# Optimization experiments

Measured on AMD Instinct MI355X. Metric: run time of the kernel, lower is better.

The kernel has to match this reference:

```python
import jax, jax.numpy as jnp
import numpy as np

B, T, V, E, H = 32, 64, 32000, 256, 512


def setup_inputs() -> dict:
    key = jax.random.key(0)
    ks = jax.random.split(key, 6)
    g = lambda k, shp, s: (jax.random.normal(k, shp, dtype=jnp.float32) * s)
    return {
        "trg": jax.random.randint(ks[0], (B, T), 0, V),
        "h0": g(ks[1], (1, B, H), 0.1),
        "embed_table": g(ks[2], (V, E), 0.02),
        "W_ih": g(ks[3], (3 * H, E), 0.05),
        "W_hh": g(ks[4], (3 * H, H), 0.05),
        "b_ih": jnp.zeros((3 * H,), jnp.float32),
        "b_hh": jnp.zeros((3 * H,), jnp.float32),
        "W_proj": g(ks[5], (V, H), 0.02),
        "b_proj": jnp.zeros((V,), jnp.float32),
    }


def _gru_decode(trg, h0, embed_table, W_ih, W_hh, b_ih, b_hh, W_proj, b_proj):
    # Teacher forcing with tf_ratio=1.0 (deterministic): token at step t is trg[:, t-1].
    Bd, Td = trg.shape
    Vd = W_proj.shape[0]
    emb = embed_table[trg[:, :-1]]                         # [B, T-1, E]
    # Precompute input-side gate projections for all steps at once.
    x_gates = jnp.einsum('bte,ge->btg', emb, W_ih) + b_ih  # [B, T-1, 3H]

    def step(h, xg):
        hg = h @ W_hh.T + b_hh                             # [B, 3H]
        xr, xz, xn = jnp.split(xg, 3, axis=-1)
        hr, hz, hn = jnp.split(hg, 3, axis=-1)
        r = jax.nn.sigmoid(xr + hr)
        z = jax.nn.sigmoid(xz + hz)
        n = jnp.tanh(xn + r * hn)
        h_new = (1.0 - z) * n + z * h                      # PyTorch GRU update
        logits = h_new @ W_proj.T + b_proj                 # [B, V]
        return h_new, jax.nn.log_softmax(logits, axis=-1)

    _, logps = jax.lax.scan(step, h0[0], jnp.swapaxes(x_gates, 0, 1))  # [T-1, B, V]
    out = jnp.concatenate(
        [jnp.zeros((Bd, 1, Vd), logps.dtype), jnp.swapaxes(logps, 0, 1)], axis=1
    )                                                      # out[:, 0] = 0 as in torch
    return out


def reference(trg, h0, embed_table, W_ih, W_hh, b_ih, b_hh, W_proj, b_proj):
    return _gru_decode(trg, h0, embed_table, W_ih, W_hh, b_ih, b_hh, W_proj, b_proj)
```

## Files before the change

### kernel.cpp

```cpp
#include <hip/hip_runtime.h>
#include <stdint.h>

#define B_  32
#define T_  64
#define V_  32000
#define E_  256
#define H_  512
#define TS  63

typedef __attribute__((ext_vector_type(8))) short short8;
typedef __attribute__((ext_vector_type(4))) float floatx4;

union U16c { uint4 u; short8 s; };

__device__ __forceinline__ short8 ld8(const unsigned short* p) {
    U16c x; x.u = *(const uint4*)p; return x.s;
}

__device__ __forceinline__ unsigned short f2bf(float f) {
    union { float f; unsigned u; } v; v.f = f;
    unsigned r = v.u + 0x7FFFu + ((v.u >> 16) & 1u);
    return (unsigned short)(r >> 16);
}

__global__ void k_cvt_wp(const float* __restrict__ wp, unsigned short* __restrict__ dst) {
    int i = blockIdx.x * blockDim.x + threadIdx.x;
    const float4* s = (const float4*)wp + (size_t)i * 2;
    float4 a = s[0], b = s[1];
    union { uint4 u; unsigned short h[8]; } o;
    o.h[0] = f2bf(a.x); o.h[1] = f2bf(a.y); o.h[2] = f2bf(a.z); o.h[3] = f2bf(a.w);
    o.h[4] = f2bf(b.x); o.h[5] = f2bf(b.y); o.h[6] = f2bf(b.z); o.h[7] = f2bf(b.w);
    ((uint4*)dst)[i] = o.u;
}

__global__ void k_setup(const float* __restrict__ wih, const float* __restrict__ whh,
                        const float* __restrict__ embt, const int* __restrict__ trg,
                        const float* __restrict__ h0,
                        unsigned short* __restrict__ wih_bf, unsigned short* __restrict__ whh_bf,
                        unsigned short* __restrict__ emb_bf, unsigned short* __restrict__ hall,
                        unsigned long long* __restrict__ hall64)
{
    const int NIH  = (3 * H_ * E_) / 4;
    const int NHH  = (3 * H_ * H_) / 4;
    const int NEMB = TS * B_ * E_ / 4;
    const int NPAD = 32 * E_ / 8;
    const int NH0  = B_ * H_ / 4;
    const int NZ   = 63 * B_ * 256 * 8 / 16;
    int i = blockIdx.x * blockDim.x + threadIdx.x;
    if (i < NIH + NHH) {
        const float* src; unsigned short* dst; int j;
        if (i < NIH) { src = wih; dst = wih_bf; j = i; }
        else         { src = whh; dst = whh_bf; j = i - NIH; }
        float4 v = ((const float4*)src)[j];
        union { unsigned long long u; unsigned short h[4]; } o;
        o.h[0] = f2bf(v.x); o.h[1] = f2bf(v.y); o.h[2] = f2bf(v.z); o.h[3] = f2bf(v.w);
        ((unsigned long long*)dst)[j] = o.u;
        return;
    }
    i -= NIH + NHH;
    if (i < NEMB) {
        int r = i >> 6, c = i & 63;
        int tt = r >> 5, b = r & 31;
        int tok = trg[b * T_ + tt];
        float4 v = ((const float4*)(embt + (size_t)tok * E_))[c];
        union { unsigned long long u; unsigned short h[4]; } o;
        o.h[0] = f2bf(v.x); o.h[1] = f2bf(v.y); o.h[2] = f2bf(v.z); o.h[3] = f2bf(v.w);
        ((unsigned long long*)(emb_bf + (size_t)r * E_))[c] = o.u;
        return;
    }
    i -= NEMB;
    if (i < NPAD) {
        uint4 z; z.x = z.y = z.z = z.w = 0u;
        ((uint4*)(emb_bf + (size_t)(TS * B_) * E_))[i] = z;
        return;
    }
    i -= NPAD;
    if (i < NH0) {
        float4 v = ((const float4*)h0)[i];
        unsigned pk01 = (unsigned)f2bf(v.x) | ((unsigned)f2bf(v.y) << 16);
        unsigned pk23 = (unsigned)f2bf(v.z) | ((unsigned)f2bf(v.w) << 16);
        union { unsigned long long u; unsigned h[2]; } o;
        o.h[0] = pk01; o.h[1] = pk23;
        ((unsigned long long*)hall)[i] = o.u;
        uint4 tw; tw.x = pk01; tw.y = 0u; tw.z = pk23; tw.w = 0u;
        ((uint4*)hall64)[i] = tw;
        return;
    }
    i -= NH0;
    if (i < NZ) {
        uint4 z; z.x = z.y = z.z = z.w = 0u;
        ((uint4*)(hall64 + (size_t)B_ * 256))[i] = z;
        return;
    }
}

__global__ __launch_bounds__(256) void k_xg(const unsigned short* __restrict__ A,
                                            const unsigned short* __restrict__ Bm,
                                            const float* __restrict__ bias,
                                            float* __restrict__ out)
{
    __shared__ unsigned short As[128 * 32];
    __shared__ unsigned short Bs[128 * 32];
    int m0 = blockIdx.x * 128, n0 = blockIdx.y * 128;
    int tid = threadIdx.x;
    int lane = tid & 63, w = tid >> 6;
    int wm = (w & 1) * 64, wn = (w >> 1) * 64;
    int row = lane & 15, quad = lane >> 4;
    int srow = lane >> 2, skc = lane & 3;
    floatx4 acc[4][4];
    #pragma unroll
    for (int a = 0; a < 4; ++a)
        #pragma unroll
        for (int b = 0; b < 4; ++b) acc[a][b] = (floatx4){0.f, 0.f, 0.f, 0.f};

    for (int k0 = 0; k0 < E_; k0 += 32) {
        if (k0) __syncthreads();
        #pragma unroll
        for (int p = 0; p < 2; ++p) {
            int seg = w * 2 + p;
            int m = seg * 16 + srow;
            __builtin_amdgcn_global_load_lds(
                (const __attribute__((address_space(1))) void*)(A + (size_t)(m0 + m) * E_ + k0 + skc * 8),
                (__attribute__((address_space(3))) void*)(As + seg * 512),
                16, 0, 0);
            __builtin_amdgcn_global_load_lds(
                (const __attribute__((address_space(1))) void*)(Bm + (size_t)(n0 + m) * E_ + k0 + skc * 8),
                (__attribute__((address_space(3))) void*)(Bs + seg * 512),
                16, 0, 0);
        }
        __syncthreads();
        short8 af[4], bf[4];
        #pragma unroll
        for (int mi2 = 0; mi2 < 4; ++mi2)
            af[mi2] = ld8(As + (wm + mi2 * 16 + row) * 32 + quad * 8);
        #pragma unroll
        for (int ni = 0; ni < 4; ++ni)
            bf[ni] = ld8(Bs + (wn + ni * 16 + row) * 32 + quad * 8);
        #pragma unroll
        for (int mi2 = 0; mi2 < 4; ++mi2)
            #pragma unroll
            for (int ni = 0; ni < 4; ++ni)
                acc[mi2][ni] = __builtin_amdgcn_mfma_f32_16x16x32_bf16(af[mi2], bf[ni], acc[mi2][ni], 0, 0, 0);
    }
    #pragma unroll
    for (int ni = 0; ni < 4; ++ni) {
        int n = n0 + wn + ni * 16 + row;
        float bp = bias[n];
        #pragma unroll
        for (int mi2 = 0; mi2 < 4; ++mi2) {
            #pragma unroll
            for (int v = 0; v < 4; ++v) {
                int m = m0 + wm + mi2 * 16 + quad * 4 + v;
                out[(size_t)m * 1536 + n] = acc[mi2][ni][v] + bp;
            }
        }
    }
}

__global__ __launch_bounds__(512) void k_gru(
    const unsigned short* __restrict__ whh_bf, const float* __restrict__ gx,
    const float* __restrict__ bhh, const float* __restrict__ h0,
    unsigned short* __restrict__ hall, unsigned long long* __restrict__ hall64)
{
    __shared__ unsigned short hs[32 * 528];
    __shared__ float gh[32][52];
    int blk = blockIdx.x, tid = threadIdx.x;
    int lane = tid & 63, w = tid >> 6;
    int mi = w & 1, gi = w >> 1;
    int row = lane & 15, quad = lane >> 4;
    int eb = tid >> 4, jl = tid & 15;
    int j = blk * 16 + jl;

    float bhhr = bhh[j], bhhz = bhh[H_ + j], bhhn = bhh[2*H_ + j];
    float hcur = h0[eb * H_ + j];

    short8 barr[16];
    if (w < 6) {
        int gr = gi * H_ + blk * 16 + row;
        const unsigned short* wrow = whh_bf + (size_t)gr * H_;
        #pragma unroll
        for (int kk = 0; kk < 16; ++kk)
            barr[kk] = ld8(wrow + kk * 32 + quad * 8);
    }

    for (int t = 0; t < TS; ++t) {
        const float* gxp = gx + (size_t)(t * B_ + eb) * 1536 + j;
        float xr = gxp[0], xz = gxp[512], xn = gxp[1024];

        const unsigned long long* src = hall64 + (size_t)t * (B_ * 256);
        unsigned long long wv[16];
        unsigned want = (unsigned)t;
        for (;;) {
            #pragma unroll
            for (int i = 0; i < 16; ++i)
                wv[i] = __hip_atomic_load(src + i * 512 + tid,
                                          __ATOMIC_RELAXED, __HIP_MEMORY_SCOPE_AGENT);
            bool ok = true;
            #pragma unroll
            for (int i = 0; i < 16; ++i) ok &= ((unsigned)(wv[i] >> 32) == want);
            if (ok) break;
        }
        #pragma unroll
        for (int i = 0; i < 16; ++i) {
            int idx = i * 512 + tid;
            ((unsigned*)(hs + (size_t)(idx >> 8) * 528))[idx & 255] = (unsigned)wv[i];
        }
        __syncthreads();

        if (w < 6) {
            floatx4 ah = {0.f, 0.f, 0.f, 0.f};
            int b_ = mi * 16 + row;
            #pragma unroll
            for (int kk = 0; kk < 16; ++kk)
                ah = __builtin_amdgcn_mfma_f32_16x16x32_bf16(
                        ld8(hs + b_ * 528 + kk * 32 + quad * 8), barr[kk], ah, 0, 0, 0);
            int cb = mi * 16 + quad * 4;
            int cn = gi * 16 + row;
            #pragma unroll
            for (int v = 0; v < 4; ++v) gh[cb + v][cn] = ah[v];
        }
        __syncthreads();
        {
            float hr = gh[eb][jl], hz = gh[eb][16 + jl], hn = gh[eb][32 + jl];
            float r = 1.f / (1.f + __expf(-(xr + hr + bhhr)));
            float z = 1.f / (1.f + __expf(-(xz + hz + bhhz)));
            float nn = tanhf(xn + r * (hn + bhhn));
            hcur = (1.f - z) * nn + z * hcur;
            float hnb = __shfl_xor(hcur, 1);
            if (!(tid & 1)) {
                unsigned pk = (unsigned)f2bf(hcur) | ((unsigned)f2bf(hnb) << 16);
                unsigned long long tw = ((unsigned long long)(unsigned)(t + 1) << 32) | pk;
                __hip_atomic_store(hall64 + ((size_t)(t + 1) * B_ + eb) * 256 + (j >> 1),
                                   tw, __ATOMIC_RELAXED, __HIP_MEMORY_SCOPE_AGENT);
                ((unsigned*)hall)[((size_t)(t + 1) * B_ + eb) * 256 + (j >> 1)] = pk;
            }
        }
    }
}

__global__ __launch_bounds__(256) void k_gemm(const unsigned short* __restrict__ A,
                                              const unsigned short* __restrict__ Bm,
                                              const float* __restrict__ bias,
                                              float* __restrict__ out)
{
    __shared__ unsigned short As[128 * 32];
    __shared__ unsigned short Bs[128 * 32];
    int m0 = blockIdx.x * 128, n0 = blockIdx.y * 128;
    int tid = threadIdx.x;
    int lane = tid & 63, w = tid >> 6;
    int wm = (w & 1) * 64, wn = (w >> 1) * 64;
    int row = lane & 15, quad = lane >> 4;
    int srow = lane >> 2, skc = lane & 3;
    floatx4 acc[4][4];
    #pragma unroll
    for (int a = 0; a < 4; ++a)
        #pragma unroll
        for (int b = 0; b < 4; ++b) acc[a][b] = (floatx4){0.f, 0.f, 0.f, 0.f};

    for (int k0 = 0; k0 < H_; k0 += 32) {
        if (k0) __syncthreads();
        #pragma unroll
        for (int p = 0; p < 2; ++p) {
            int seg = w * 2 + p;
            int m = seg * 16 + srow;
            __builtin_amdgcn_global_load_lds(
                (const __attribute__((address_space(1))) void*)(A + (size_t)(m0 + m) * H_ + k0 + skc * 8),
                (__attribute__((address_space(3))) void*)(As + seg * 512),
                16, 0, 0);
            __builtin_amdgcn_global_load_lds(
                (const __attribute__((address_space(1))) void*)(Bm + (size_t)(n0 + m) * H_ + k0 + skc * 8),
                (__attribute__((address_space(3))) void*)(Bs + seg * 512),
                16, 0, 0);
        }
        __syncthreads();
        short8 af[4], bf[4];
        #pragma unroll
        for (int mi2 = 0; mi2 < 4; ++mi2)
            af[mi2] = ld8(As + (wm + mi2 * 16 + row) * 32 + quad * 8);
        #pragma unroll
        for (int ni = 0; ni < 4; ++ni)
            bf[ni] = ld8(Bs + (wn + ni * 16 + row) * 32 + quad * 8);
        #pragma unroll
        for (int mi2 = 0; mi2 < 4; ++mi2)
            #pragma unroll
            for (int ni = 0; ni < 4; ++ni)
                acc[mi2][ni] = __builtin_amdgcn_mfma_f32_16x16x32_bf16(af[mi2], bf[ni], acc[mi2][ni], 0, 0, 0);
    }
    #pragma unroll
    for (int ni = 0; ni < 4; ++ni) {
        int n = n0 + wn + ni * 16 + row;
        float bp = bias[n];
        #pragma unroll
        for (int mi2 = 0; mi2 < 4; ++mi2) {
            #pragma unroll
            for (int v = 0; v < 4; ++v) {
                int m = m0 + wm + mi2 * 16 + quad * 4 + v;
                int orow = (m & 31) * 64 + (m >> 5);
                out[(size_t)orow * V_ + n] = acc[mi2][ni][v] + bp;
            }
        }
    }
}

__global__ __launch_bounds__(320) void k_lsm(float* __restrict__ out)
{
    __shared__ float red[5];
    int rown = blockIdx.x;
    int t = rown & 63;
    float4* p = (float4*)(out + (size_t)rown * V_);
    int tid = threadIdx.x;
    if (t == 0) {
        float4 z; z.x = z.y = z.z = z.w = 0.f;
        for (int i = tid; i < V_ / 4; i += 320) p[i] = z;
        return;
    }
    float4 v[25];
    #pragma unroll
    for (int jj = 0; jj < 25; ++jj) v[jj] = p[tid + jj * 320];
    float m = -3.4e38f;
    #pragma unroll
    for (int jj = 0; jj < 25; ++jj)
        m = fmaxf(m, fmaxf(fmaxf(v[jj].x, v[jj].y), fmaxf(v[jj].z, v[jj].w)));
    #pragma unroll
    for (int o = 32; o > 0; o >>= 1) m = fmaxf(m, __shfl_xor(m, o));
    if ((tid & 63) == 0) red[tid >> 6] = m;
    __syncthreads();
    m = fmaxf(fmaxf(fmaxf(red[0], red[1]), fmaxf(red[2], red[3])), red[4]);
    __syncthreads();
    float s = 0.f;
    #pragma unroll
    for (int jj = 0; jj < 25; ++jj)
        s += __expf(v[jj].x - m) + __expf(v[jj].y - m) + __expf(v[jj].z - m) + __expf(v[jj].w - m);
    #pragma unroll
    for (int o = 32; o > 0; o >>= 1) s += __shfl_xor(s, o);
    if ((tid & 63) == 0) red[tid >> 6] = s;
    __syncthreads();
    s = red[0] + red[1] + red[2] + red[3] + red[4];
    float lz = m + logf(s);
    #pragma unroll
    for (int jj = 0; jj < 25; ++jj) {
        float4 o4;
        o4.x = v[jj].x - lz; o4.y = v[jj].y - lz; o4.z = v[jj].z - lz; o4.w = v[jj].w - lz;
        p[tid + jj * 320] = o4;
    }
}

extern "C" void kernel_launch(void* const* d_in, const int* in_sizes, int n_in,
                              void* d_out, int out_size, void* d_ws, size_t ws_size,
                              hipStream_t stream) {
    const int*   trg   = (const int*)d_in[0];
    const float* h0    = (const float*)d_in[1];
    const float* embt  = (const float*)d_in[2];
    const float* wih   = (const float*)d_in[3];
    const float* whh   = (const float*)d_in[4];
    const float* bih   = (const float*)d_in[5];
    const float* bhh   = (const float*)d_in[6];
    const float* wproj = (const float*)d_in[7];
    const float* bproj = (const float*)d_in[8];
    float* out = (float*)d_out;

    char* ws = (char*)d_ws;
    size_t off = 0;
    unsigned short* wp_bf  = (unsigned short*)(ws + off); off += (size_t)V_ * H_ * 2;
    unsigned short* wih_bf = (unsigned short*)(ws + off); off += (size_t)3 * H_ * E_ * 2;
    unsigned short* whh_bf = (unsigned short*)(ws + off); off += (size_t)3 * H_ * H_ * 2;
    unsigned short* emb_bf = (unsigned short*)(ws + off); off += (size_t)64 * B_ * E_ * 2;
    unsigned short* hall   = (unsigned short*)(ws + off); off += (size_t)64 * B_ * H_ * 2;
    float*              gx     = (float*)d_out;
    unsigned long long* hall64 = (unsigned long long*)((char*)d_out + (size_t)16 * 1024 * 1024);

    k_cvt_wp<<<8000, 256, 0, stream>>>(wproj, wp_bf);
    k_setup<<<2684, 256, 0, stream>>>(wih, whh, embt, trg, h0,
                                      wih_bf, whh_bf, emb_bf, hall, hall64);
    dim3 xg(16, 12);
    k_xg<<<xg, 256, 0, stream>>>(emb_bf, wih_bf, bih, gx);
    k_gru<<<32, 512, 0, stream>>>(whh_bf, gx, bhh, h0, hall, hall64);
    dim3 gg(16, 250);
    k_gemm<<<gg, 256, 0, stream>>>(hall, wp_bf, bproj, out);
    k_lsm<<<2048, 320, 0, stream>>>(out);
}
```

Baseline: 687.4 us.

## Fuse GRU recurrence and vocab projection GEMM into one persistent kernel

```diff
diff --git a/kernel.cpp b/kernel.cpp
--- a/kernel.cpp
+++ b/kernel.cpp
@@ -37,7 +37,7 @@
                         const float* __restrict__ embt, const int* __restrict__ trg,
                         const float* __restrict__ h0,
                         unsigned short* __restrict__ wih_bf, unsigned short* __restrict__ whh_bf,
-                        unsigned short* __restrict__ emb_bf, unsigned short* __restrict__ hall,
+                        unsigned short* __restrict__ emb_bf,
                         unsigned long long* __restrict__ hall64)
 {
     const int NIH  = (3 * H_ * E_) / 4;
@@ -79,9 +79,6 @@
         float4 v = ((const float4*)h0)[i];
         unsigned pk01 = (unsigned)f2bf(v.x) | ((unsigned)f2bf(v.y) << 16);
         unsigned pk23 = (unsigned)f2bf(v.z) | ((unsigned)f2bf(v.w) << 16);
-        union { unsigned long long u; unsigned h[2]; } o;
-        o.h[0] = pk01; o.h[1] = pk23;
-        ((unsigned long long*)hall)[i] = o.u;
         uint4 tw; tw.x = pk01; tw.y = 0u; tw.z = pk23; tw.w = 0u;
         ((uint4*)hall64)[i] = tw;
         return;
@@ -157,146 +154,172 @@
     }
 }
 
-__global__ __launch_bounds__(512) void k_gru(
+__global__ __launch_bounds__(512) void k_fused(
     const unsigned short* __restrict__ whh_bf, const float* __restrict__ gx,
     const float* __restrict__ bhh, const float* __restrict__ h0,
-    unsigned short* __restrict__ hall, unsigned long long* __restrict__ hall64)
+    unsigned long long* __restrict__ hall64,
+    const unsigned short* __restrict__ wp_bf, const float* __restrict__ bias,
+    float* __restrict__ out)
 {
-    __shared__ unsigned short hs[32 * 528];
-    __shared__ float gh[32][52];
+    __shared__ __align__(16) char smem[40448];
     int blk = blockIdx.x, tid = threadIdx.x;
     int lane = tid & 63, w = tid >> 6;
-    int mi = w & 1, gi = w >> 1;
-    int row = lane & 15, quad = lane >> 4;
-    int eb = tid >> 4, jl = tid & 15;
-    int j = blk * 16 + jl;
-
-    float bhhr = bhh[j], bhhz = bhh[H_ + j], bhhn = bhh[2*H_ + j];
-    float hcur = h0[eb * H_ + j];
-
-    short8 barr[16];
-    if (w < 6) {
-        int gr = gi * H_ + blk * 16 + row;
-        const unsigned short* wrow = whh_bf + (size_t)gr * H_;
-        #pragma unroll
-        for (int kk = 0; kk < 16; ++kk)
-            barr[kk] = ld8(wrow + kk * 32 + quad * 8);
-    }
-
-    for (int t = 0; t < TS; ++t) {
-        const float* gxp = gx + (size_t)(t * B_ + eb) * 1536 + j;
-        float xr = gxp[0], xz = gxp[512], xn = gxp[1024];
-
-        const unsigned long long* src = hall64 + (size_t)t * (B_ * 256);
-        unsigned long long wv[16];
-        unsigned want = (unsigned)t;
-        for (;;) {
-            #pragma unroll
-            for (int i = 0; i < 16; ++i)
-                wv[i] = __hip_atomic_load(src + i * 512 + tid,
-                                          __ATOMIC_RELAXED, __HIP_MEMORY_SCOPE_AGENT);
-            bool ok = true;
-            #pragma unroll
-            for (int i = 0; i < 16; ++i) ok &= ((unsigned)(wv[i] >> 32) == want);
-            if (ok) break;
+
+    if (blk < 32) {
+        unsigned short* hs = (unsigned short*)smem;
+        float (*gh)[52] = (float(*)[52])(smem + 33792);
+        int mi = w & 1, gi = w >> 1;
+        int row = lane & 15, quad = lane >> 4;
+        int eb = tid >> 4, jl = tid & 15;
+        int j = blk * 16 + jl;
+
+        float bhhr = bhh[j], bhhz = bhh[H_ + j], bhhn = bhh[2*H_ + j];
+        float hcur = h0[eb * H_ + j];
+
+        short8 barr[16];
+        if (w < 6) {
+            int gr = gi * H_ + blk * 16 + row;
+            const unsigned short* wrow = whh_bf + (size_t)gr * H_;
+            #pragma unroll
+            for (int kk = 0; kk < 16; ++kk)
+                barr[kk] = ld8(wrow + kk * 32 + quad * 8);
         }
-        #pragma unroll
-        for (int i = 0; i < 16; ++i) {
-            int idx = i * 512 + tid;
-            ((unsigned*)(hs + (size_t)(idx >> 8) * 528))[idx & 255] = (unsigned)wv[i];
+
+        for (int t = 0; t < TS; ++t) {
+            const float* gxp = gx + (size_t)(t * B_ + eb) * 1536 + j;
+            float xr = gxp[0], xz = gxp[512], xn = gxp[1024];
+
+            const unsigned long long* src = hall64 + (size_t)t * (B_ * 256);
+            unsigned long long wv[16];
+            unsigned want = (unsigned)t;
+            for (;;) {
+                #pragma unroll
+                for (int i = 0; i < 16; ++i)
+                    wv[i] = __hip_atomic_load(src + i * 512 + tid,
+                                              __ATOMIC_RELAXED, __HIP_MEMORY_SCOPE_AGENT);
+                bool ok = true;
+                #pragma unroll
+                for (int i = 0; i < 16; ++i) ok &= ((unsigned)(wv[i] >> 32) == want);
+                if (ok) break;
+            }
+            #pragma unroll
+            for (int i = 0; i < 16; ++i) {
+                int idx = i * 512 + tid;
+                ((unsigned*)(hs + (size_t)(idx >> 8) * 528))[idx & 255] = (unsigned)wv[i];
+            }
+            __syncthreads();
+
+            if (w < 6) {
+                floatx4 ah = {0.f, 0.f, 0.f, 0.f};
+                int b_ = mi * 16 + row;
+                #pragma unroll
+                for (int kk = 0; kk < 16; ++kk)
+                    ah = __builtin_amdgcn_mfma_f32_16x16x32_bf16(
+                            ld8(hs + b_ * 528 + kk * 32 + quad * 8), barr[kk], ah, 0, 0, 0);
+                int cb = mi * 16 + quad * 4;
+                int cn = gi * 16 + row;
+                #pragma unroll
+                for (int v = 0; v < 4; ++v) gh[cb + v][cn] = ah[v];
+            }
+            __syncthreads();
+            {
+                float hr = gh[eb][jl], hz = gh[eb][16 + jl], hn = gh[eb][32 + jl];
+                float r = 1.f / (1.f + __expf(-(xr + hr + bhhr)));
+                float z = 1.f / (1.f + __expf(-(xz + hz + bhhz)));
+                float nn = tanhf(xn + r * (hn + bhhn));
+                hcur = (1.f - z) * nn + z * hcur;
+                float hnb = __shfl_xor(hcur, 1);
+                if (!(tid & 1)) {
+                    unsigned pk = (unsigned)f2bf(hcur) | ((unsigned)f2bf(hnb) << 16);
+                    unsigned long long tw = ((unsigned long long)(unsigned)(t + 1) << 32) | pk;
+                    __hip_atomic_store(hall64 + ((size_t)(t + 1) * B_ + eb) * 256 + (j >> 1),
+                                       tw, __ATOMIC_RELAXED, __HIP_MEMORY_SCOPE_AGENT);
+                }
+            }
         }
-        __syncthreads();
-
-        if (w < 6) {
-            floatx4 ah = {0.f, 0.f, 0.f, 0.f};
-            int b_ = mi * 16 + row;
-            #pragma unroll
-            for (int kk = 0; kk < 16; ++kk)
-                ah = __builtin_amdgcn_mfma_f32_16x16x32_bf16(
-                        ld8(hs + b_ * 528 + kk * 32 + quad * 8), barr[kk], ah, 0, 0, 0);
-            int cb = mi * 16 + quad * 4;
-            int cn = gi * 16 + row;
-            #pragma unroll
-            for (int v = 0; v < 4; ++v) gh[cb + v][cn] = ah[v];
-        }
-        __syncthreads();
-        {
-            float hr = gh[eb][jl], hz = gh[eb][16 + jl], hn = gh[eb][32 + jl];
-            float r = 1.f / (1.f + __expf(-(xr + hr + bhhr)));
-            float z = 1.f / (1.f + __expf(-(xz + hz + bhhz)));
-            float nn = tanhf(xn + r * (hn + bhhn));
-            hcur = (1.f - z) * nn + z * hcur;
-            float hnb = __shfl_xor(hcur, 1);
-            if (!(tid & 1)) {
-                unsigned pk = (unsigned)f2bf(hcur) | ((unsigned)f2bf(hnb) << 16);
-                unsigned long long tw = ((unsigned long long)(unsigned)(t + 1) << 32) | pk;
-                __hip_atomic_store(hall64 + ((size_t)(t + 1) * B_ + eb) * 256 + (j >> 1),
-                                   tw, __ATOMIC_RELAXED, __HIP_MEMORY_SCOPE_AGENT);
-                ((unsigned*)hall)[((size_t)(t + 1) * B_ + eb) * 256 + (j >> 1)] = pk;
-            }
-        }
-    }
-}
-
-__global__ __launch_bounds__(256) void k_gemm(const unsigned short* __restrict__ A,
-                                              const unsigned short* __restrict__ Bm,
-                                              const float* __restrict__ bias,
-                                              float* __restrict__ out)
-{
-    __shared__ unsigned short As[128 * 32];
-    __shared__ unsigned short Bs[128 * 32];
-    int m0 = blockIdx.x * 128, n0 = blockIdx.y * 128;
-    int tid = threadIdx.x;
-    int lane = tid & 63, w = tid >> 6;
-    int wm = (w & 1) * 64, wn = (w >> 1) * 64;
-    int row = lane & 15, quad = lane >> 4;
-    int srow = lane >> 2, skc = lane & 3;
-    floatx4 acc[4][4];
-    #pragma unroll
-    for (int a = 0; a < 4; ++a)
-        #pragma unroll
-        for (int b = 0; b < 4; ++b) acc[a][b] = (floatx4){0.f, 0.f, 0.f, 0.f};
-
-    for (int k0 = 0; k0 < H_; k0 += 32) {
-        if (k0) __syncthreads();
-        #pragma unroll
-        for (int p = 0; p < 2; ++p) {
-            int seg = w * 2 + p;
-            int m = seg * 16 + srow;
-            __builtin_amdgcn_global_load_lds(
-                (const __attribute__((address_space(1))) void*)(A + (size_t)(m0 + m) * H_ + k0 + skc * 8),
-                (__attribute__((address_space(3))) void*)(As + seg * 512),
-                16, 0, 0);
-            __builtin_amdgcn_global_load_lds(
-                (const __attribute__((address_space(1))) void*)(Bm + (size_t)(n0 + m) * H_ + k0 + skc * 8),
-                (__attribute__((address_space(3))) void*)(Bs + seg * 512),
-                16, 0, 0);
-        }
-        __syncthreads();
-        short8 af[4], bf[4];
-        #pragma unroll
-        for (int mi2 = 0; mi2 < 4; ++mi2)
-            af[mi2] = ld8(As + (wm + mi2 * 16 + row) * 32 + quad * 8);
-        #pragma unroll
-        for (int ni = 0; ni < 4; ++ni)
-            bf[ni] = ld8(Bs + (wn + ni * 16 + row) * 32 + quad * 8);
-        #pragma unroll
-        for (int mi2 = 0; mi2 < 4; ++mi2)
-            #pragma unroll
-            for (int ni = 0; ni < 4; ++ni)
-                acc[mi2][ni] = __builtin_amdgcn_mfma_f32_16x16x32_bf16(af[mi2], bf[ni], acc[mi2][ni], 0, 0, 0);
-    }
-    #pragma unroll
-    for (int ni = 0; ni < 4; ++ni) {
-        int n = n0 + wn + ni * 16 + row;
-        float bp = bias[n];
-        #pragma unroll
-        for (int mi2 = 0; mi2 < 4; ++mi2) {
-            #pragma unroll
-            for (int v = 0; v < 4; ++v) {
-                int m = m0 + wm + mi2 * 16 + quad * 4 + v;
-                int orow = (m & 31) * 64 + (m >> 5);
-                out[(size_t)orow * V_ + n] = acc[mi2][ni][v] + bp;
+    } else {
+        unsigned short* As = (unsigned short*)smem;
+        unsigned short* Bs = (unsigned short*)(smem + 8192);
+        int g = blk - 32;
+        int wm = (w & 1) * 64, wn = (w >> 1) * 64;
+        int row16 = lane & 15, quad = lane >> 4;
+        int srow = lane >> 2, skc = lane & 3;
+
+        for (int T = g; T < 2000; T += 224) {
+            int mx = T / 125, ny = T - mx * 125;
+            int m0 = mx * 128, n0 = ny * 256;
+            if (tid == 0) {
+                const unsigned long long* gate = hall64 + (size_t)(4 * mx + 3) * 32 * 256;
+                while ((unsigned)(__hip_atomic_load(gate, __ATOMIC_RELAXED,
+                                                    __HIP_MEMORY_SCOPE_AGENT) >> 32)
+                       != (unsigned)(4 * mx + 3))
+                    __builtin_amdgcn_s_sleep(32);
+            }
+
+            floatx4 acc[4][4];
+            #pragma unroll
+            for (int a = 0; a < 4; ++a)
+                #pragma unroll
+                for (int b = 0; b < 4; ++b) acc[a][b] = (floatx4){0.f, 0.f, 0.f, 0.f};
+
+            for (int k0 = 0; k0 < H_; k0 += 32) {
+                __syncthreads();
+                #pragma unroll
+                for (int p = 0; p < 2; ++p) {
+                    int seg = w * 2 + p;
+                    int r = seg * 16 + srow;
+                    __builtin_amdgcn_global_load_lds(
+                        (const __attribute__((address_space(1))) void*)(wp_bf + (size_t)(n0 + r) * H_ + k0 + skc * 8),
+                        (__attribute__((address_space(3))) void*)(Bs + seg * 512),
+                        16, 0, 0);
+                }
+                unsigned long long av[4];
+                #pragma unroll
+                for (int i = 0; i < 4; ++i) {
+                    int idx = i * 512 + tid;
+                    av[i] = __hip_atomic_load(
+                        hall64 + (size_t)(m0 + (idx >> 4)) * 256 + (k0 >> 1) + (idx & 15),
+                        __ATOMIC_RELAXED, __HIP_MEMORY_SCOPE_AGENT);
+                }
+                #pragma unroll
+                for (int i = 0; i < 4; ++i) {
+                    int idx = i * 512 + tid;
+                    int R = m0 + (idx >> 4);
+                    unsigned want = (unsigned)(R >> 5);
+                    while ((unsigned)(av[i] >> 32) != want)
+                        av[i] = __hip_atomic_load(
+                            hall64 + (size_t)R * 256 + (k0 >> 1) + (idx & 15),
+                            __ATOMIC_RELAXED, __HIP_MEMORY_SCOPE_AGENT);
+                    ((unsigned*)As)[idx] = (unsigned)av[i];
+                }
+                __syncthreads();
+                short8 af[4], bfr[4];
+                #pragma unroll
+                for (int mi2 = 0; mi2 < 4; ++mi2)
+                    af[mi2] = ld8(As + (wm + mi2 * 16 + row16) * 32 + quad * 8);
+                #pragma unroll
+                for (int ni = 0; ni < 4; ++ni)
+                    bfr[ni] = ld8(Bs + (wn + ni * 16 + row16) * 32 + quad * 8);
+                #pragma unroll
+                for (int mi2 = 0; mi2 < 4; ++mi2)
+                    #pragma unroll
+                    for (int ni = 0; ni < 4; ++ni)
+                        acc[mi2][ni] = __builtin_amdgcn_mfma_f32_16x16x32_bf16(
+                                           af[mi2], bfr[ni], acc[mi2][ni], 0, 0, 0);
+            }
+            #pragma unroll
+            for (int ni = 0; ni < 4; ++ni) {
+                int n = n0 + wn + ni * 16 + row16;
+                float bp = bias[n];
+                #pragma unroll
+                for (int mi2 = 0; mi2 < 4; ++mi2) {
+                    #pragma unroll
+                    for (int v = 0; v < 4; ++v) {
+                        int m = m0 + wm + mi2 * 16 + quad * 4 + v;
+                        int orow = (m & 31) * 64 + (m >> 5);
+                        out[(size_t)orow * V_ + n] = acc[mi2][ni][v] + bp;
+                    }
+                }
             }
         }
     }
@@ -365,17 +388,14 @@
     unsigned short* wih_bf = (unsigned short*)(ws + off); off += (size_t)3 * H_ * E_ * 2;
     unsigned short* whh_bf = (unsigned short*)(ws + off); off += (size_t)3 * H_ * H_ * 2;
     unsigned short* emb_bf = (unsigned short*)(ws + off); off += (size_t)64 * B_ * E_ * 2;
-    unsigned short* hall   = (unsigned short*)(ws + off); off += (size_t)64 * B_ * H_ * 2;
-    float*              gx     = (float*)d_out;
-    unsigned long long* hall64 = (unsigned long long*)((char*)d_out + (size_t)16 * 1024 * 1024);
+    float*              gx = (float*)(ws + off);          off += (size_t)2048 * 1536 * 4;
+    unsigned long long* hall64 = (unsigned long long*)(ws + off); off += (size_t)64 * B_ * 256 * 8;
 
     k_cvt_wp<<<8000, 256, 0, stream>>>(wproj, wp_bf);
     k_setup<<<2684, 256, 0, stream>>>(wih, whh, embt, trg, h0,
-                                      wih_bf, whh_bf, emb_bf, hall, hall64);
+                                      wih_bf, whh_bf, emb_bf, hall64);
     dim3 xg(16, 12);
     k_xg<<<xg, 256, 0, stream>>>(emb_bf, wih_bf, bih, gx);
-    k_gru<<<32, 512, 0, stream>>>(whh_bf, gx, bhh, h0, hall, hall64);
-    dim3 gg(16, 250);
-    k_gemm<<<gg, 256, 0, stream>>>(hall, wp_bf, bproj, out);
+    k_fused<<<256, 512, 0, stream>>>(whh_bf, gx, bhh, h0, hall64, wp_bf, bproj, out);
     k_lsm<<<2048, 320, 0, stream>>>(out);
 }
```

Result: faster. 653.4 us (-5.0%).
